# Kernel tuning notes

Hardware: AMD Instinct MI355X
Metric: run time of the kernel (lower is better)

The kernel has to match this reference:

```python
import jax, jax.numpy as jnp
import numpy as np

N = 50000
E = 600000
IN_F = 12
HID = 64
HEADS = 8
NUM_CLASSES = 3
NEG_SLOPE = 0.2


def _glorot(key, shape):
    fan_in, fan_out = shape[0], shape[-1]
    lim = np.sqrt(6.0 / (fan_in + fan_out))
    return jax.random.uniform(key, shape, jnp.float32, -lim, lim)


def setup_inputs() -> dict:
    key = jax.random.key(0)
    ks = jax.random.split(key, 16)
    x = jax.random.normal(ks[0], (N, IN_F), jnp.float32)
    edge_index = jax.random.randint(ks[1], (2, E), 0, N, jnp.int32)
    d = {
        "x": x,
        "edge_index": edge_index,
        "W1": _glorot(ks[2], (IN_F, HEADS * HID)),
        "asrc1": _glorot(ks[3], (HEADS, HID)),
        "adst1": _glorot(ks[4], (HEADS, HID)),
        "b1": jnp.zeros((HEADS * HID,), jnp.float32),
        "W2": _glorot(ks[5], (HEADS * HID, HEADS * HID)),
        "asrc2": _glorot(ks[6], (HEADS, HID)),
        "adst2": _glorot(ks[7], (HEADS, HID)),
        "b2": jnp.zeros((HEADS * HID,), jnp.float32),
        # layer 3: 512 -> 3, single head, averaged
        "W3": _glorot(ks[8], (HEADS * HID, NUM_CLASSES)),
        "asrc3": _glorot(ks[9], (1, NUM_CLASSES)),
        "adst3": _glorot(ks[10], (1, NUM_CLASSES)),
        "b3": jnp.zeros((NUM_CLASSES,), jnp.float32),
    }
    return d


def gat_conv(x, src, dst, W, a_src, a_dst, b, heads, out_ch, concat):
    # x: (N, F_in); src/dst: (E',) with self-loops already appended
    n = x.shape[0]
    h = (x @ W).reshape(n, heads, out_ch)            # (N, H, C)
    alpha_src = jnp.sum(h * a_src, axis=-1)          # (N, H)
    alpha_dst = jnp.sum(h * a_dst, axis=-1)          # (N, H)
    e = alpha_src[src] + alpha_dst[dst]              # (E', H)
    e = jax.nn.leaky_relu(e, NEG_SLOPE)
    # segment softmax over destination nodes
    emax = jax.ops.segment_max(e, dst, num_segments=n)
    emax = jnp.where(jnp.isfinite(emax), emax, 0.0)
    ex = jnp.exp(e - emax[dst])
    denom = jax.ops.segment_sum(ex, dst, num_segments=n)
    alpha = ex / (denom[dst] + 1e-16)                # (E', H)
    msg = h[src] * alpha[:, :, None]                 # (E', H, C)
    out = jax.ops.segment_sum(msg, dst, num_segments=n)  # (N, H, C)
    if concat:
        out = out.reshape(n, heads * out_ch)
    else:
        out = out.mean(axis=1)
    return out + b


def reference(x, edge_index, W1, asrc1, adst1, b1, W2, asrc2, adst2, b2, W3, asrc3, adst3, b3):
    n = x.shape[0]
    loops = jnp.arange(n, dtype=edge_index.dtype)
    src = jnp.concatenate([edge_index[0], loops])
    dst = jnp.concatenate([edge_index[1], loops])
    # eval mode: dropout is identity
    h = gat_conv(x, src, dst, W1, asrc1, adst1, b1, HEADS, HID, True)
    h = jax.nn.elu(h)
    h = gat_conv(h, src, dst, W2, asrc2, adst2, b2, HEADS, HID, True)
    h = jax.nn.elu(h)
    logits = gat_conv(h, src, dst, W3, asrc3, adst3, b3, 1, NUM_CLASSES, False)
    return logits
```

## Files before the change

### kernel.cpp

```cpp
#include <hip/hip_runtime.h>
#include <hip/hip_bf16.h>
#include <hip/hip_fp16.h>


#define HEADS 8
#define HID 64
#define F512 512

typedef __bf16 bf16x8 __attribute__((ext_vector_type(8)));
typedef unsigned short u16x8 __attribute__((ext_vector_type(8)));
typedef float f32x4 __attribute__((ext_vector_type(4)));

__device__ __forceinline__ unsigned bf16_rne(float f) {
    unsigned u = __float_as_uint(f);
    return (u + 0x7FFFu + ((u >> 16) & 1u)) >> 16;
}
__device__ __forceinline__ unsigned pack_split(float f) {
    unsigned hi = bf16_rne(f);
    float r = f - __uint_as_float(hi << 16);
    unsigned lo = bf16_rne(r);
    return hi | (lo << 16);
}

__global__ __launch_bounds__(256) void gemm1_fused(
    const float* __restrict__ x, const float* __restrict__ W1,
    const float* __restrict__ asrc, const float* __restrict__ adst,
    __half* __restrict__ h16, float* __restrict__ a_s, float* __restrict__ a_d,
    int N) {
    int w = (blockIdx.x * blockDim.x + threadIdx.x) >> 6;
    int l = threadIdx.x & 63;
    if (w >= N) return;
    const float* xr = x + (size_t)w * 12;
    float4 xa = *(const float4*)(xr);
    float4 xb = *(const float4*)(xr + 4);
    float4 xc = *(const float4*)(xr + 8);
    float xv[12] = {xa.x, xa.y, xa.z, xa.w, xb.x, xb.y, xb.z, xb.w, xc.x, xc.y, xc.z, xc.w};
    int c0 = l * 8;
    float o[8] = {};
#pragma unroll
    for (int k = 0; k < 12; ++k) {
        const float4* wr = (const float4*)(W1 + k * F512 + c0);
        float4 w0 = wr[0], w1 = wr[1];
        o[0] += xv[k] * w0.x; o[1] += xv[k] * w0.y; o[2] += xv[k] * w0.z; o[3] += xv[k] * w0.w;
        o[4] += xv[k] * w1.x; o[5] += xv[k] * w1.y; o[6] += xv[k] * w1.z; o[7] += xv[k] * w1.w;
    }
    __half hv[8];
#pragma unroll
    for (int k = 0; k < 8; ++k) hv[k] = __float2half_rn(o[k]);
    *(uint4*)(h16 + (size_t)w * F512 + c0) = *(uint4*)hv;
    float s = 0.f, d = 0.f;
#pragma unroll
    for (int k = 0; k < 8; ++k) { s += o[k] * asrc[c0 + k]; d += o[k] * adst[c0 + k]; }
    s += __shfl_xor(s, 1); d += __shfl_xor(d, 1);
    s += __shfl_xor(s, 2); d += __shfl_xor(d, 2);
    s += __shfl_xor(s, 4); d += __shfl_xor(d, 4);
    if ((l & 7) == 0) { a_s[w * 8 + (l >> 3)] = s; a_d[w * 8 + (l >> 3)] = d; }
}

__global__ void convW2_kernel(const float* __restrict__ W2, unsigned* __restrict__ BT) {
    int tid = blockIdx.x * blockDim.x + threadIdx.x;
    if (tid >= F512 * F512) return;
    int n = tid & 511, k = tid >> 9;
    BT[(size_t)n * F512 + k] = pack_split(W2[(size_t)k * F512 + n]);
}

__global__ __launch_bounds__(256) void gemm2_mfma(
    const unsigned* __restrict__ Ap, const unsigned* __restrict__ BT,
    const float* __restrict__ asrc2, const float* __restrict__ adst2,
    __half* __restrict__ C, float* __restrict__ a_s, float* __restrict__ a_d,
    int M) {
    __shared__ unsigned short AsH[128 * 32], AsL[128 * 32];
    __shared__ unsigned short BsH[128 * 32], BsL[128 * 32];

    int nwg = gridDim.x;
    int o = blockIdx.x;
    int q = nwg >> 3, r = nwg & 7, xcd = o & 7;
    int base = xcd < r ? xcd * (q + 1) : r * (q + 1) + (xcd - r) * q;
    int lg = base + (o >> 3);
    int mb = lg >> 2, nb = lg & 3;

    int tid = threadIdx.x;
    int lane = tid & 63, wv = tid >> 6;
    int wm = wv >> 1, wn = wv & 1;
    int srow = tid >> 2, schunk = tid & 3;
    int seg = lane >> 4;

    f32x4 acc[4][4] = {};

    for (int k0 = 0; k0 < F512; k0 += 32) {
#pragma unroll
        for (int u = 0; u < 2; ++u) {
            int rr = srow + u * 64;
            int off = rr * 32 + ((schunk ^ ((rr >> 1) & 3)) << 3);
            {
                const uint4* g = (const uint4*)(Ap + ((size_t)(mb * 128 + rr)) * F512 + k0 + schunk * 8);
                uint4 g0 = g[0], g1 = g[1];
                uint4 hi, lo;
                hi.x = (g0.x & 0xFFFFu) | (g0.y << 16); lo.x = (g0.x >> 16) | (g0.y & 0xFFFF0000u);
                hi.y = (g0.z & 0xFFFFu) | (g0.w << 16); lo.y = (g0.z >> 16) | (g0.w & 0xFFFF0000u);
                hi.z = (g1.x & 0xFFFFu) | (g1.y << 16); lo.z = (g1.x >> 16) | (g1.y & 0xFFFF0000u);
                hi.w = (g1.z & 0xFFFFu) | (g1.w << 16); lo.w = (g1.z >> 16) | (g1.w & 0xFFFF0000u);
                *(uint4*)&AsH[off] = hi;
                *(uint4*)&AsL[off] = lo;
            }
            {
                const uint4* g = (const uint4*)(BT + ((size_t)(nb * 128 + rr)) * F512 + k0 + schunk * 8);
                uint4 g0 = g[0], g1 = g[1];
                uint4 hi, lo;
                hi.x = (g0.x & 0xFFFFu) | (g0.y << 16); lo.x = (g0.x >> 16) | (g0.y & 0xFFFF0000u);
                hi.y = (g0.z & 0xFFFFu) | (g0.w << 16); lo.y = (g0.z >> 16) | (g0.w & 0xFFFF0000u);
                hi.z = (g1.x & 0xFFFFu) | (g1.y << 16); lo.z = (g1.x >> 16) | (g1.y & 0xFFFF0000u);
                hi.w = (g1.z & 0xFFFFu) | (g1.w << 16); lo.w = (g1.z >> 16) | (g1.w & 0xFFFF0000u);
                *(uint4*)&BsH[off] = hi;
                *(uint4*)&BsL[off] = lo;
            }
        }
        __syncthreads();

        bf16x8 aH[4], aL[4], bH[4], bL[4];
#pragma unroll
        for (int mi = 0; mi < 4; ++mi) {
            int arow = wm * 64 + mi * 16 + (lane & 15);
            int aoff = arow * 32 + ((seg ^ ((arow >> 1) & 3)) << 3);
            aH[mi] = __builtin_bit_cast(bf16x8, *(const u16x8*)&AsH[aoff]);
            aL[mi] = __builtin_bit_cast(bf16x8, *(const u16x8*)&AsL[aoff]);
        }
#pragma unroll
        for (int ni = 0; ni < 4; ++ni) {
            int brow = wn * 64 + ni * 16 + (lane & 15);
            int boff = brow * 32 + ((seg ^ ((brow >> 1) & 3)) << 3);
            bH[ni] = __builtin_bit_cast(bf16x8, *(const u16x8*)&BsH[boff]);
            bL[ni] = __builtin_bit_cast(bf16x8, *(const u16x8*)&BsL[boff]);
        }
#pragma unroll
        for (int mi = 0; mi < 4; ++mi)
#pragma unroll
            for (int ni = 0; ni < 4; ++ni) {
                acc[mi][ni] = __builtin_amdgcn_mfma_f32_16x16x32_bf16(aH[mi], bH[ni], acc[mi][ni], 0, 0, 0);
                acc[mi][ni] = __builtin_amdgcn_mfma_f32_16x16x32_bf16(aH[mi], bL[ni], acc[mi][ni], 0, 0, 0);
                acc[mi][ni] = __builtin_amdgcn_mfma_f32_16x16x32_bf16(aL[mi], bH[ni], acc[mi][ni], 0, 0, 0);
            }
        __syncthreads();
    }

#pragma unroll
    for (int mi = 0; mi < 4; ++mi) {
#pragma unroll
        for (int ni = 0; ni < 4; ++ni) {
            int rbase = mb * 128 + wm * 64 + mi * 16 + (lane >> 4) * 4;
            int c = nb * 128 + wn * 64 + ni * 16 + (lane & 15);
#pragma unroll
            for (int i = 0; i < 4; ++i) {
                int row = rbase + i;
                if (row < M) C[(size_t)row * F512 + c] = __float2half_rn(acc[mi][ni][i]);
            }
        }
    }

    int head = nb * 2 + wn;
    float av[4], dv[4];
#pragma unroll
    for (int ni = 0; ni < 4; ++ni) {
        int cw = ni * 16 + (lane & 15);
        av[ni] = asrc2[head * 64 + cw];
        dv[ni] = adst2[head * 64 + cw];
    }
#pragma unroll
    for (int mi = 0; mi < 4; ++mi)
#pragma unroll
        for (int i = 0; i < 4; ++i) {
            float sp = 0.f, dp = 0.f;
#pragma unroll
            for (int ni = 0; ni < 4; ++ni) {
                sp += acc[mi][ni][i] * av[ni];
                dp += acc[mi][ni][i] * dv[ni];
            }
            sp += __shfl_xor(sp, 1); dp += __shfl_xor(dp, 1);
            sp += __shfl_xor(sp, 2); dp += __shfl_xor(dp, 2);
            sp += __shfl_xor(sp, 4); dp += __shfl_xor(dp, 4);
            sp += __shfl_xor(sp, 8); dp += __shfl_xor(dp, 8);
            if ((lane & 15) == 0) {
                int row = mb * 128 + wm * 64 + mi * 16 + (lane >> 4) * 4 + i;
                if (row < M) { a_s[row * 8 + head] = sp; a_d[row * 8 + head] = dp; }
            }
        }
}


__global__ void hist_kernel(const int* __restrict__ dst, int E, int* __restrict__ cnt) {
    int e = blockIdx.x * blockDim.x + threadIdx.x;
    if (e < E) atomicAdd(&cnt[dst[e]], 1);
}

__global__ __launch_bounds__(1024) void scan_block_kernel(const int* __restrict__ cnt,
                                                          int* __restrict__ excl,
                                                          int* __restrict__ bsum, int n) {
    __shared__ int s[1024];
    int i = blockIdx.x * 1024 + threadIdx.x;
    int v = i < n ? cnt[i] : 0;
    s[threadIdx.x] = v;
    __syncthreads();
    for (int off = 1; off < 1024; off <<= 1) {
        int t = threadIdx.x >= off ? s[threadIdx.x - off] : 0;
        __syncthreads();
        s[threadIdx.x] += t;
        __syncthreads();
    }
    if (i < n) excl[i] = s[threadIdx.x] - v;
    if (threadIdx.x == 1023) bsum[blockIdx.x] = s[1023];
}

__global__ void scan_aux_kernel(int* __restrict__ bsum, int nb) {
    if (blockIdx.x == 0 && threadIdx.x == 0) {
        int acc = 0;
        for (int i = 0; i < nb; ++i) { int v = bsum[i]; bsum[i] = acc; acc += v; }
    }
}

__global__ void scan_add_kernel(const int* __restrict__ excl, const int* __restrict__ bsum,
                                int* __restrict__ rowptr, int* __restrict__ fill, int n, int E) {
    int i = blockIdx.x * blockDim.x + threadIdx.x;
    if (i < n) {
        int v = excl[i] + bsum[i >> 10];
        rowptr[i] = v;
        fill[i] = v;
    }
    if (i == 0) rowptr[n] = E;
}

__global__ void scatter_kernel(const int* __restrict__ src, const int* __restrict__ dst, int E,
                               int* __restrict__ fill, int* __restrict__ csrc) {
    int e = blockIdx.x * blockDim.x + threadIdx.x;
    if (e >= E) return;
    int pos = atomicAdd(&fill[dst[e]], 1);
    csrc[pos] = src[e];
}


template <int MODE>
__global__ __launch_bounds__(256) void gat_aggr_wave(
    const int* __restrict__ rowptr, const int* __restrict__ csrc,
    const float* __restrict__ a_s, const float* __restrict__ a_d,
    const __half* __restrict__ h16, const float* __restrict__ bias,
    unsigned* __restrict__ outp,
    const float* __restrict__ W3, const float* __restrict__ asrc3,
    const float* __restrict__ adst3, float* __restrict__ h3,
    float* __restrict__ as3, float* __restrict__ ad3, int N) {
    __shared__ float sexs[4][64 * 8];
    __shared__ int ssrcs[4][64];
    int wv = threadIdx.x >> 6, l = threadIdx.x & 63;
    int d = blockIdx.x * 4 + wv;
    if (d >= N) return;
    float* SX = sexs[wv];
    int* SS = ssrcs[wv];
    int beg = rowptr[d], deg = rowptr[d + 1] - beg;
    int hq = l & 7, hmy = l >> 3;
    float adq = a_d[d * 8 + hq];

    float m = -INFINITY;
    for (int i = l >> 3; i <= deg; i += 8) {
        int s = (i == deg) ? d : csrc[beg + i];
        float v = a_s[s * 8 + hq] + adq;
        v = v >= 0.f ? v : 0.2f * v;
        m = fmaxf(m, v);
    }
    m = fmaxf(m, __shfl_xor(m, 8));
    m = fmaxf(m, __shfl_xor(m, 16));
    m = fmaxf(m, __shfl_xor(m, 32));

    float den = 0.f;
    float acc[8] = {};
    for (int c0 = 0; c0 <= deg; c0 += 64) {
        int cnt = min(64, deg + 1 - c0);
        if (l < cnt) {
            int i = c0 + l;
            SS[l] = (i == deg) ? d : csrc[beg + i];
        }
        __builtin_amdgcn_wave_barrier();
        for (int i = l >> 3; i < cnt; i += 8) {
            int s = SS[i];
            float v = a_s[s * 8 + hq] + adq;
            v = v >= 0.f ? v : 0.2f * v;
            float ex = __expf(v - m);
            SX[i * 8 + hq] = ex;
            den += ex;
        }
        __builtin_amdgcn_wave_barrier();
        for (int j = 0; j < cnt; ++j) {
            int s = SS[j];
            float ex = SX[j * 8 + hmy];
            uint4 hv = *(const uint4*)(h16 + (size_t)s * F512 + l * 8);
            const __half2* hp = (const __half2*)&hv;
#pragma unroll
            for (int k = 0; k < 4; ++k) {
                float2 f = __half22float2(hp[k]);
                acc[2 * k] += ex * f.x;
                acc[2 * k + 1] += ex * f.y;
            }
        }
        __builtin_amdgcn_wave_barrier();
    }
    den += __shfl_xor(den, 8);
    den += __shfl_xor(den, 16);
    den += __shfl_xor(den, 32);
    float dg = __shfl(den, hmy);
    float inv = 1.f / (dg + 1e-16f);

    int c0c = l * 8;
    float o[8];
#pragma unroll
    for (int k = 0; k < 8; ++k) {
        float t = acc[k] * inv + bias[c0c + k];
        o[k] = t > 0.f ? t : expm1f(t);
    }

    if (MODE == 0) {
        unsigned pk[8];
#pragma unroll
        for (int k = 0; k < 8; ++k) pk[k] = pack_split(o[k]);
        uint4* op = (uint4*)(outp + (size_t)d * F512 + c0c);
        op[0] = *(uint4*)&pk[0];
        op[1] = *(uint4*)&pk[4];
    } else {
        float p0 = 0.f, p1 = 0.f, p2 = 0.f;
#pragma unroll
        for (int k = 0; k < 8; ++k) {
            float t = o[k];
            p0 += t * W3[(c0c + k) * 3 + 0];
            p1 += t * W3[(c0c + k) * 3 + 1];
            p2 += t * W3[(c0c + k) * 3 + 2];
        }
#pragma unroll
        for (int off = 1; off < 64; off <<= 1) {
            p0 += __shfl_xor(p0, off);
            p1 += __shfl_xor(p1, off);
            p2 += __shfl_xor(p2, off);
        }
        if (l == 0) {
            h3[(size_t)d * 3 + 0] = p0;
            h3[(size_t)d * 3 + 1] = p1;
            h3[(size_t)d * 3 + 2] = p2;
            as3[d] = p0 * asrc3[0] + p1 * asrc3[1] + p2 * asrc3[2];
            ad3[d] = p0 * adst3[0] + p1 * adst3[1] + p2 * adst3[2];
        }
    }
}

__global__ __launch_bounds__(256) void gat_aggr3_fused(
    const int* __restrict__ rowptr, const int* __restrict__ csrc,
    const float* __restrict__ a_s, const float* __restrict__ a_d,
    const float* __restrict__ h3, const float* __restrict__ b3,
    float* __restrict__ out, int N) {
    int w = (blockIdx.x * blockDim.x + threadIdx.x) >> 6;
    int lane = threadIdx.x & 63;
    if (w >= N) return;
    int d = w;
    int beg = rowptr[d], deg = rowptr[d + 1] - beg;
    float ad = a_d[d];
    float m = -INFINITY;
    for (int i = lane; i <= deg; i += 64) {
        int s = (i == deg) ? d : csrc[beg + i];
        float v = a_s[s] + ad;
        v = v >= 0.f ? v : 0.2f * v;
        m = fmaxf(m, v);
    }
    for (int off = 32; off; off >>= 1) m = fmaxf(m, __shfl_xor(m, off));
    float den = 0.f, c0 = 0.f, c1 = 0.f, c2 = 0.f;
    for (int i = lane; i <= deg; i += 64) {
        int s = (i == deg) ? d : csrc[beg + i];
        float v = a_s[s] + ad;
        v = v >= 0.f ? v : 0.2f * v;
        float ex = __expf(v - m);
        den += ex;
        c0 += ex * h3[(size_t)s * 3 + 0];
        c1 += ex * h3[(size_t)s * 3 + 1];
        c2 += ex * h3[(size_t)s * 3 + 2];
    }
    for (int off = 32; off; off >>= 1) {
        den += __shfl_xor(den, off);
        c0 += __shfl_xor(c0, off);
        c1 += __shfl_xor(c1, off);
        c2 += __shfl_xor(c2, off);
    }
    if (lane == 0) {
        float inv = 1.f / (den + 1e-16f);
        out[(size_t)d * 3 + 0] = c0 * inv + b3[0];
        out[(size_t)d * 3 + 1] = c1 * inv + b3[1];
        out[(size_t)d * 3 + 2] = c2 * inv + b3[2];
    }
}

static inline int cdiv(long long a, long long b) { return (int)((a + b - 1) / b); }
static inline size_t rup(size_t v) { return (v + 255) & ~(size_t)255; }

extern "C" void kernel_launch(void* const* d_in, const int* in_sizes, int n_in,
                              void* d_out, int out_size, void* d_ws, size_t ws_size,
                              hipStream_t stream) {
    const int N = in_sizes[0] / 12;
    const int E = in_sizes[1] / 2;
    const float* x     = (const float*)d_in[0];
    const int*   ei    = (const int*)d_in[1];
    const float* W1    = (const float*)d_in[2];
    const float* asrc1 = (const float*)d_in[3];
    const float* adst1 = (const float*)d_in[4];
    const float* b1    = (const float*)d_in[5];
    const float* W2    = (const float*)d_in[6];
    const float* asrc2 = (const float*)d_in[7];
    const float* adst2 = (const float*)d_in[8];
    const float* b2    = (const float*)d_in[9];
    const float* W3    = (const float*)d_in[10];
    const float* asrc3 = (const float*)d_in[11];
    const float* adst3 = (const float*)d_in[12];
    const float* b3    = (const float*)d_in[13];

    const int* srcv = ei;
    const int* dstv = ei + E;
    float* out = (float*)d_out;

    const int Mpad = cdiv(N, 128) * 128;
    char* ws = (char*)d_ws;
    size_t szH16 = rup((size_t)Mpad * F512 * 2);
    size_t szHp  = rup((size_t)Mpad * F512 * 4);
    __half*   h16 = (__half*)ws;
    unsigned* hBp = (unsigned*)(ws + szH16);
    char* p = ws + szH16 + szHp;
    float* a_s    = (float*)p;  p += rup((size_t)Mpad * HEADS * 4);
    float* a_d    = (float*)p;  p += rup((size_t)Mpad * HEADS * 4);
    float* h3     = (float*)p;  p += rup((size_t)N * 3 * 4);
    float* as3    = (float*)p;  p += rup((size_t)N * 4);
    float* ad3    = (float*)p;  p += rup((size_t)N * 4);
    int*   cnt    = (int*)p;    p += rup((size_t)N * 4);
    int*   excl   = (int*)p;    p += rup((size_t)N * 4);
    int*   rowptr = (int*)p;    p += rup((size_t)(N + 1) * 4);
    int*   fill   = (int*)p;    p += rup((size_t)N * 4);
    int*   bsum   = (int*)p;    p += rup(4096);
    int*   csrc   = (int*)p;    p += rup((size_t)E * 4);
    unsigned* BT  = (unsigned*)p;

    const int nb = cdiv(N, 1024);

    hipMemsetAsync(cnt, 0, (size_t)N * 4, stream);
    hist_kernel<<<cdiv(E, 256), 256, 0, stream>>>(dstv, E, cnt);
    scan_block_kernel<<<nb, 1024, 0, stream>>>(cnt, excl, bsum, N);
    scan_aux_kernel<<<1, 64, 0, stream>>>(bsum, nb);
    scan_add_kernel<<<cdiv(N + 1, 256), 256, 0, stream>>>(excl, bsum, rowptr, fill, N, E);
    scatter_kernel<<<cdiv(E, 256), 256, 0, stream>>>(srcv, dstv, E, fill, csrc);
    convW2_kernel<<<cdiv((long long)F512 * F512, 256), 256, 0, stream>>>(W2, BT);

    gemm1_fused<<<cdiv((long long)N * 64, 256), 256, 0, stream>>>(
        x, W1, asrc1, adst1, h16, a_s, a_d, N);
    gat_aggr_wave<0><<<cdiv(N, 4), 256, 0, stream>>>(
        rowptr, csrc, a_s, a_d, h16, b1, hBp,
        nullptr, nullptr, nullptr, nullptr, nullptr, nullptr, N);

    gemm2_mfma<<<(Mpad / 128) * 4, 256, 0, stream>>>(
        hBp, BT, asrc2, adst2, h16, a_s, a_d, N);
    gat_aggr_wave<1><<<cdiv(N, 4), 256, 0, stream>>>(
        rowptr, csrc, a_s, a_d, h16, b2, nullptr,
        W3, asrc3, adst3, h3, as3, ad3, N);

    gat_aggr3_fused<<<cdiv((long long)N, 4), 256, 0, stream>>>(
        rowptr, csrc, as3, ad3, h3, b3, out, N);
}
```

Baseline: 511.6 us.

## Pre-split and pre-swizzle GEMM2 operands, load via global_load_lds

The layer-1 aggregation now writes its output as separate hi and lo bf16 planes, and the W2 conversion writes separate planes too. Both are stored in the pre-swizzled per-32-column chunk layout the GEMM reads from LDS. The second GEMM then copies tiles straight from global memory into LDS with the global_load_lds builtin, skipping the register round trip and the per-tile hi/lo unpacking. The risk is that the producer-side swizzle must exactly match the LDS lane placement of the direct loads. Padding rows in aggH/aggL are never written, though they only feed output rows that are skipped.

```diff
diff --git a/kernel.cpp b/kernel.cpp
--- a/kernel.cpp
+++ b/kernel.cpp
@@ -4,7 +4,6 @@
 
 
 #define HEADS 8
-#define HID 64
 #define F512 512
 
 typedef __bf16 bf16x8 __attribute__((ext_vector_type(8)));
@@ -15,11 +14,21 @@
     unsigned u = __float_as_uint(f);
     return (u + 0x7FFFu + ((u >> 16) & 1u)) >> 16;
 }
-__device__ __forceinline__ unsigned pack_split(float f) {
-    unsigned hi = bf16_rne(f);
-    float r = f - __uint_as_float(hi << 16);
-    unsigned lo = bf16_rne(r);
-    return hi | (lo << 16);
+
+#if defined(__has_builtin)
+#if __has_builtin(__builtin_amdgcn_global_load_lds)
+#define HAS_GLL 1
+#endif
+#endif
+
+__device__ __forceinline__ void gll16(const void* g, void* l) {
+#ifdef HAS_GLL
+    __builtin_amdgcn_global_load_lds(
+        (const __attribute__((address_space(1))) unsigned int*)g,
+        (__attribute__((address_space(3))) unsigned int*)l, 16, 0, 0);
+#else
+    *(uint4*)l = *(const uint4*)g;
+#endif
 }
 
 __global__ __launch_bounds__(256) void gemm1_fused(
@@ -57,133 +66,24 @@
     if ((l & 7) == 0) { a_s[w * 8 + (l >> 3)] = s; a_d[w * 8 + (l >> 3)] = d; }
 }
 
-__global__ void convW2_kernel(const float* __restrict__ W2, unsigned* __restrict__ BT) {
-    int tid = blockIdx.x * blockDim.x + threadIdx.x;
-    if (tid >= F512 * F512) return;
-    int n = tid & 511, k = tid >> 9;
-    BT[(size_t)n * F512 + k] = pack_split(W2[(size_t)k * F512 + n]);
-}
-
-__global__ __launch_bounds__(256) void gemm2_mfma(
-    const unsigned* __restrict__ Ap, const unsigned* __restrict__ BT,
-    const float* __restrict__ asrc2, const float* __restrict__ adst2,
-    __half* __restrict__ C, float* __restrict__ a_s, float* __restrict__ a_d,
-    int M) {
-    __shared__ unsigned short AsH[128 * 32], AsL[128 * 32];
-    __shared__ unsigned short BsH[128 * 32], BsL[128 * 32];
-
-    int nwg = gridDim.x;
-    int o = blockIdx.x;
-    int q = nwg >> 3, r = nwg & 7, xcd = o & 7;
-    int base = xcd < r ? xcd * (q + 1) : r * (q + 1) + (xcd - r) * q;
-    int lg = base + (o >> 3);
-    int mb = lg >> 2, nb = lg & 3;
-
-    int tid = threadIdx.x;
-    int lane = tid & 63, wv = tid >> 6;
-    int wm = wv >> 1, wn = wv & 1;
-    int srow = tid >> 2, schunk = tid & 3;
-    int seg = lane >> 4;
-
-    f32x4 acc[4][4] = {};
-
-    for (int k0 = 0; k0 < F512; k0 += 32) {
-#pragma unroll
-        for (int u = 0; u < 2; ++u) {
-            int rr = srow + u * 64;
-            int off = rr * 32 + ((schunk ^ ((rr >> 1) & 3)) << 3);
-            {
-                const uint4* g = (const uint4*)(Ap + ((size_t)(mb * 128 + rr)) * F512 + k0 + schunk * 8);
-                uint4 g0 = g[0], g1 = g[1];
-                uint4 hi, lo;
-                hi.x = (g0.x & 0xFFFFu) | (g0.y << 16); lo.x = (g0.x >> 16) | (g0.y & 0xFFFF0000u);
-                hi.y = (g0.z & 0xFFFFu) | (g0.w << 16); lo.y = (g0.z >> 16) | (g0.w & 0xFFFF0000u);
-                hi.z = (g1.x & 0xFFFFu) | (g1.y << 16); lo.z = (g1.x >> 16) | (g1.y & 0xFFFF0000u);
-                hi.w = (g1.z & 0xFFFFu) | (g1.w << 16); lo.w = (g1.z >> 16) | (g1.w & 0xFFFF0000u);
-                *(uint4*)&AsH[off] = hi;
-                *(uint4*)&AsL[off] = lo;
-            }
-            {
-                const uint4* g = (const uint4*)(BT + ((size_t)(nb * 128 + rr)) * F512 + k0 + schunk * 8);
-                uint4 g0 = g[0], g1 = g[1];
-                uint4 hi, lo;
-                hi.x = (g0.x & 0xFFFFu) | (g0.y << 16); lo.x = (g0.x >> 16) | (g0.y & 0xFFFF0000u);
-                hi.y = (g0.z & 0xFFFFu) | (g0.w << 16); lo.y = (g0.z >> 16) | (g0.w & 0xFFFF0000u);
-                hi.z = (g1.x & 0xFFFFu) | (g1.y << 16); lo.z = (g1.x >> 16) | (g1.y & 0xFFFF0000u);
-                hi.w = (g1.z & 0xFFFFu) | (g1.w << 16); lo.w = (g1.z >> 16) | (g1.w & 0xFFFF0000u);
-                *(uint4*)&BsH[off] = hi;
-                *(uint4*)&BsL[off] = lo;
-            }
-        }
-        __syncthreads();
-
-        bf16x8 aH[4], aL[4], bH[4], bL[4];
-#pragma unroll
-        for (int mi = 0; mi < 4; ++mi) {
-            int arow = wm * 64 + mi * 16 + (lane & 15);
-            int aoff = arow * 32 + ((seg ^ ((arow >> 1) & 3)) << 3);
-            aH[mi] = __builtin_bit_cast(bf16x8, *(const u16x8*)&AsH[aoff]);
-            aL[mi] = __builtin_bit_cast(bf16x8, *(const u16x8*)&AsL[aoff]);
-        }
-#pragma unroll
-        for (int ni = 0; ni < 4; ++ni) {
-            int brow = wn * 64 + ni * 16 + (lane & 15);
-            int boff = brow * 32 + ((seg ^ ((brow >> 1) & 3)) << 3);
-            bH[ni] = __builtin_bit_cast(bf16x8, *(const u16x8*)&BsH[boff]);
-            bL[ni] = __builtin_bit_cast(bf16x8, *(const u16x8*)&BsL[boff]);
-        }
-#pragma unroll
-        for (int mi = 0; mi < 4; ++mi)
-#pragma unroll
-            for (int ni = 0; ni < 4; ++ni) {
-                acc[mi][ni] = __builtin_amdgcn_mfma_f32_16x16x32_bf16(aH[mi], bH[ni], acc[mi][ni], 0, 0, 0);
-                acc[mi][ni] = __builtin_amdgcn_mfma_f32_16x16x32_bf16(aH[mi], bL[ni], acc[mi][ni], 0, 0, 0);
-                acc[mi][ni] = __builtin_amdgcn_mfma_f32_16x16x32_bf16(aL[mi], bH[ni], acc[mi][ni], 0, 0, 0);
-            }
-        __syncthreads();
-    }
-
-#pragma unroll
-    for (int mi = 0; mi < 4; ++mi) {
-#pragma unroll
-        for (int ni = 0; ni < 4; ++ni) {
-            int rbase = mb * 128 + wm * 64 + mi * 16 + (lane >> 4) * 4;
-            int c = nb * 128 + wn * 64 + ni * 16 + (lane & 15);
-#pragma unroll
-            for (int i = 0; i < 4; ++i) {
-                int row = rbase + i;
-                if (row < M) C[(size_t)row * F512 + c] = __float2half_rn(acc[mi][ni][i]);
-            }
-        }
-    }
-
-    int head = nb * 2 + wn;
-    float av[4], dv[4];
-#pragma unroll
-    for (int ni = 0; ni < 4; ++ni) {
-        int cw = ni * 16 + (lane & 15);
-        av[ni] = asrc2[head * 64 + cw];
-        dv[ni] = adst2[head * 64 + cw];
-    }
-#pragma unroll
-    for (int mi = 0; mi < 4; ++mi)
-#pragma unroll
-        for (int i = 0; i < 4; ++i) {
-            float sp = 0.f, dp = 0.f;
-#pragma unroll
-            for (int ni = 0; ni < 4; ++ni) {
-                sp += acc[mi][ni][i] * av[ni];
-                dp += acc[mi][ni][i] * dv[ni];
-            }
-            sp += __shfl_xor(sp, 1); dp += __shfl_xor(dp, 1);
-            sp += __shfl_xor(sp, 2); dp += __shfl_xor(dp, 2);
-            sp += __shfl_xor(sp, 4); dp += __shfl_xor(dp, 4);
-            sp += __shfl_xor(sp, 8); dp += __shfl_xor(dp, 8);
-            if ((lane & 15) == 0) {
-                int row = mb * 128 + wm * 64 + mi * 16 + (lane >> 4) * 4 + i;
-                if (row < M) { a_s[row * 8 + head] = sp; a_d[row * 8 + head] = dp; }
-            }
-        }
+__global__ void convW2p(const float* __restrict__ W2, unsigned short* __restrict__ BTH,
+                        unsigned short* __restrict__ BTL) {
+    int t = blockIdx.x * blockDim.x + threadIdx.x;
+    if (t >= F512 * 64) return;
+    int n = t >> 6, c = t & 63;
+    int g = c >> 2, cc = c & 3;
+    int st = g * 32 + ((cc ^ ((n >> 1) & 3)) << 3);
+    unsigned short hs[8], ls[8];
+#pragma unroll
+    for (int j = 0; j < 8; ++j) {
+        float f = W2[(size_t)(c * 8 + j) * F512 + n];
+        unsigned hi = bf16_rne(f);
+        float r = f - __uint_as_float(hi << 16);
+        hs[j] = (unsigned short)hi;
+        ls[j] = (unsigned short)bf16_rne(r);
+    }
+    *(uint4*)&BTH[(size_t)n * F512 + st] = *(uint4*)hs;
+    *(uint4*)&BTL[(size_t)n * F512 + st] = *(uint4*)ls;
 }
 
 
@@ -242,7 +142,7 @@
     const int* __restrict__ rowptr, const int* __restrict__ csrc,
     const float* __restrict__ a_s, const float* __restrict__ a_d,
     const __half* __restrict__ h16, const float* __restrict__ bias,
-    unsigned* __restrict__ outp,
+    unsigned short* __restrict__ aggH, unsigned short* __restrict__ aggL,
     const float* __restrict__ W3, const float* __restrict__ asrc3,
     const float* __restrict__ adst3, float* __restrict__ h3,
     float* __restrict__ as3, float* __restrict__ ad3, int N) {
@@ -315,12 +215,17 @@
     }
 
     if (MODE == 0) {
-        unsigned pk[8];
-#pragma unroll
-        for (int k = 0; k < 8; ++k) pk[k] = pack_split(o[k]);
-        uint4* op = (uint4*)(outp + (size_t)d * F512 + c0c);
-        op[0] = *(uint4*)&pk[0];
-        op[1] = *(uint4*)&pk[4];
+        unsigned short hs[8], ls[8];
+#pragma unroll
+        for (int k = 0; k < 8; ++k) {
+            unsigned hi = bf16_rne(o[k]);
+            float r = o[k] - __uint_as_float(hi << 16);
+            hs[k] = (unsigned short)hi;
+            ls[k] = (unsigned short)bf16_rne(r);
+        }
+        int st = (l >> 2) * 32 + (((l & 3) ^ ((d >> 1) & 3)) << 3);
+        *(uint4*)&aggH[(size_t)d * F512 + st] = *(uint4*)hs;
+        *(uint4*)&aggL[(size_t)d * F512 + st] = *(uint4*)ls;
     } else {
         float p0 = 0.f, p1 = 0.f, p2 = 0.f;
 #pragma unroll
@@ -344,6 +249,110 @@
             ad3[d] = p0 * adst3[0] + p1 * adst3[1] + p2 * adst3[2];
         }
     }
+}
+
+__global__ __launch_bounds__(256) void gemm2_gll(
+    const unsigned short* __restrict__ AH, const unsigned short* __restrict__ AL,
+    const unsigned short* __restrict__ BH, const unsigned short* __restrict__ BL,
+    const float* __restrict__ asrc2, const float* __restrict__ adst2,
+    __half* __restrict__ C, float* __restrict__ a_s, float* __restrict__ a_d,
+    int M) {
+    __shared__ unsigned short AsH[128 * 32], AsL[128 * 32];
+    __shared__ unsigned short BsH[128 * 32], BsL[128 * 32];
+
+    int nwg = gridDim.x, o = blockIdx.x;
+    int q = nwg >> 3, r = nwg & 7, xcd = o & 7;
+    int base = xcd < r ? xcd * (q + 1) : r * (q + 1) + (xcd - r) * q;
+    int lg = base + (o >> 3);
+    int mb = lg >> 2, nb = lg & 3;
+
+    int tid = threadIdx.x, lane = tid & 63, wv = tid >> 6;
+    int wm = wv >> 1, wn = wv & 1;
+    int seg = lane >> 4;
+    int srow = tid >> 2, sch = tid & 3;
+
+    f32x4 acc[4][4] = {};
+
+    for (int k0 = 0; k0 < F512; k0 += 32) {
+#pragma unroll
+        for (int u = 0; u < 2; ++u) {
+            size_t ga = (size_t)(mb * 128 + srow + u * 64) * F512 + k0 + sch * 8;
+            size_t gb = (size_t)(nb * 128 + srow + u * 64) * F512 + k0 + sch * 8;
+            int ldst = wv * 512 + u * 2048;
+            gll16(AH + ga, &AsH[ldst]);
+            gll16(AL + ga, &AsL[ldst]);
+            gll16(BH + gb, &BsH[ldst]);
+            gll16(BL + gb, &BsL[ldst]);
+        }
+        __syncthreads();
+
+        bf16x8 aH[4], aL[4], bH[4], bL[4];
+#pragma unroll
+        for (int mi = 0; mi < 4; ++mi) {
+            int arow = wm * 64 + mi * 16 + (lane & 15);
+            int aoff = arow * 32 + ((seg ^ ((arow >> 1) & 3)) << 3);
+            aH[mi] = __builtin_bit_cast(bf16x8, *(const u16x8*)&AsH[aoff]);
+            aL[mi] = __builtin_bit_cast(bf16x8, *(const u16x8*)&AsL[aoff]);
+        }
+#pragma unroll
+        for (int ni = 0; ni < 4; ++ni) {
+            int brow = wn * 64 + ni * 16 + (lane & 15);
+            int boff = brow * 32 + ((seg ^ ((brow >> 1) & 3)) << 3);
+            bH[ni] = __builtin_bit_cast(bf16x8, *(const u16x8*)&BsH[boff]);
+            bL[ni] = __builtin_bit_cast(bf16x8, *(const u16x8*)&BsL[boff]);
+        }
+#pragma unroll
+        for (int mi = 0; mi < 4; ++mi)
+#pragma unroll
+            for (int ni = 0; ni < 4; ++ni) {
+                acc[mi][ni] = __builtin_amdgcn_mfma_f32_16x16x32_bf16(aH[mi], bH[ni], acc[mi][ni], 0, 0, 0);
+                acc[mi][ni] = __builtin_amdgcn_mfma_f32_16x16x32_bf16(aH[mi], bL[ni], acc[mi][ni], 0, 0, 0);
+                acc[mi][ni] = __builtin_amdgcn_mfma_f32_16x16x32_bf16(aL[mi], bH[ni], acc[mi][ni], 0, 0, 0);
+            }
+        __syncthreads();
+    }
+
+#pragma unroll
+    for (int mi = 0; mi < 4; ++mi) {
+#pragma unroll
+        for (int ni = 0; ni < 4; ++ni) {
+            int rbase = mb * 128 + wm * 64 + mi * 16 + (lane >> 4) * 4;
+            int c = nb * 128 + wn * 64 + ni * 16 + (lane & 15);
+#pragma unroll
+            for (int i = 0; i < 4; ++i) {
+                int row = rbase + i;
+                if (row < M) C[(size_t)row * F512 + c] = __float2half_rn(acc[mi][ni][i]);
+            }
+        }
+    }
+
+    int head = nb * 2 + wn;
+    float av[4], dv[4];
+#pragma unroll
+    for (int ni = 0; ni < 4; ++ni) {
+        int cw = ni * 16 + (lane & 15);
+        av[ni] = asrc2[head * 64 + cw];
+        dv[ni] = adst2[head * 64 + cw];
+    }
+#pragma unroll
+    for (int mi = 0; mi < 4; ++mi)
+#pragma unroll
+        for (int i = 0; i < 4; ++i) {
+            float sp = 0.f, dp = 0.f;
+#pragma unroll
+            for (int ni = 0; ni < 4; ++ni) {
+                sp += acc[mi][ni][i] * av[ni];
+                dp += acc[mi][ni][i] * dv[ni];
+            }
+            sp += __shfl_xor(sp, 1); dp += __shfl_xor(dp, 1);
+            sp += __shfl_xor(sp, 2); dp += __shfl_xor(dp, 2);
+            sp += __shfl_xor(sp, 4); dp += __shfl_xor(dp, 4);
+            sp += __shfl_xor(sp, 8); dp += __shfl_xor(dp, 8);
+            if ((lane & 15) == 0) {
+                int row = mb * 128 + wm * 64 + mi * 16 + (lane >> 4) * 4 + i;
+                if (row < M) { a_s[row * 8 + head] = sp; a_d[row * 8 + head] = dp; }
+            }
+        }
 }
 
 __global__ __launch_bounds__(256) void gat_aggr3_fused(
@@ -418,12 +427,10 @@
     float* out = (float*)d_out;
 
     const int Mpad = cdiv(N, 128) * 128;
-    char* ws = (char*)d_ws;
-    size_t szH16 = rup((size_t)Mpad * F512 * 2);
-    size_t szHp  = rup((size_t)Mpad * F512 * 4);
-    __half*   h16 = (__half*)ws;
-    unsigned* hBp = (unsigned*)(ws + szH16);
-    char* p = ws + szH16 + szHp;
+    char* p = (char*)d_ws;
+    __half*         h16  = (__half*)p;         p += rup((size_t)N * F512 * 2);
+    unsigned short* aggH = (unsigned short*)p; p += rup((size_t)Mpad * F512 * 2);
+    unsigned short* aggL = (unsigned short*)p; p += rup((size_t)Mpad * F512 * 2);
     float* a_s    = (float*)p;  p += rup((size_t)Mpad * HEADS * 4);
     float* a_d    = (float*)p;  p += rup((size_t)Mpad * HEADS * 4);
     float* h3     = (float*)p;  p += rup((size_t)N * 3 * 4);
@@ -435,7 +442,8 @@
     int*   fill   = (int*)p;    p += rup((size_t)N * 4);
     int*   bsum   = (int*)p;    p += rup(4096);
     int*   csrc   = (int*)p;    p += rup((size_t)E * 4);
-    unsigned* BT  = (unsigned*)p;
+    unsigned short* BTH = (unsigned short*)p; p += rup((size_t)F512 * F512 * 2);
+    unsigned short* BTL = (unsigned short*)p; p += rup((size_t)F512 * F512 * 2);
 
     const int nb = cdiv(N, 1024);
 
@@ -445,18 +453,18 @@
     scan_aux_kernel<<<1, 64, 0, stream>>>(bsum, nb);
     scan_add_kernel<<<cdiv(N + 1, 256), 256, 0, stream>>>(excl, bsum, rowptr, fill, N, E);
     scatter_kernel<<<cdiv(E, 256), 256, 0, stream>>>(srcv, dstv, E, fill, csrc);
-    convW2_kernel<<<cdiv((long long)F512 * F512, 256), 256, 0, stream>>>(W2, BT);
+    convW2p<<<cdiv(F512 * 64, 256), 256, 0, stream>>>(W2, BTH, BTL);
 
     gemm1_fused<<<cdiv((long long)N * 64, 256), 256, 0, stream>>>(
         x, W1, asrc1, adst1, h16, a_s, a_d, N);
     gat_aggr_wave<0><<<cdiv(N, 4), 256, 0, stream>>>(
-        rowptr, csrc, a_s, a_d, h16, b1, hBp,
+        rowptr, csrc, a_s, a_d, h16, b1, aggH, aggL,
         nullptr, nullptr, nullptr, nullptr, nullptr, nullptr, N);
 
-    gemm2_mfma<<<(Mpad / 128) * 4, 256, 0, stream>>>(
-        hBp, BT, asrc2, adst2, h16, a_s, a_d, N);
+    gemm2_gll<<<(Mpad / 128) * 4, 256, 0, stream>>>(
+        aggH, aggL, BTH, BTL, asrc2, adst2, h16, a_s, a_d, N);
     gat_aggr_wave<1><<<cdiv(N, 4), 256, 0, stream>>>(
-        rowptr, csrc, a_s, a_d, h16, b2, nullptr,
+        rowptr, csrc, a_s, a_d, h16, b2, nullptr, nullptr,
         W3, asrc3, adst3, h3, as3, ad3, N);
 
     gat_aggr3_fused<<<cdiv((long long)N, 4), 256, 0, stream>>>(
```

Result: no change. 502.1 us (-1.9%).
